# Optimization experiments

Hardware: AMD Instinct MI355X
Metric: run time of the kernel (lower is better)

The kernel has to match this reference:

```python
import jax, jax.numpy as jnp
import numpy as np

INF = 1e6  # stands in for +infinity in the distance transform (fp32-safe when squared)


def _edt(sites):
    """Exact Euclidean distance to the nearest True pixel.
    sites: bool [N, H, W] -> float32 [N, H, W].
    Pass 1: exact 1D distance along width via min-plus cumulative scans.
    Pass 2: lower envelope over rows, d2[y] = min_y' (g[y']^2 + (y-y')^2),
    computed row-by-row with lax.map to avoid an [N,H,W,H] intermediate.
    """
    N, H, W = sites.shape
    pen = jnp.where(sites, 0.0, INF).astype(jnp.float32)  # 0 at sites, INF elsewhere
    xs = jnp.arange(W, dtype=jnp.float32)
    # d_fwd[i] = min_{j<=i} (i - j + pen[j]);  d_bwd[i] = min_{j>=i} (j - i + pen[j])
    fwd = xs + jax.lax.cummin(pen - xs, axis=2)
    bwd = -xs + jax.lax.cummin(pen + xs, axis=2, reverse=True)
    g = jnp.minimum(fwd, bwd)  # exact 1D distance along width
    g2 = g * g
    ys = jnp.arange(H, dtype=jnp.float32)

    def row_min(y):
        # min over source row y' of g2[:, y', :] + (y - y')^2  -> [N, W]
        return jnp.min(g2 + ((y - ys) ** 2)[None, :, None], axis=1)

    d2 = jax.lax.map(row_min, ys)  # [H, N, W]
    return jnp.sqrt(jnp.transpose(d2, (1, 0, 2)))


def _phi(mask):
    """Signed level-set function: -dist_inside on foreground, +dist_outside on background.
    mask: bool [B, H, W]. Images with empty foreground get all-zero phi (as in the torch code).
    """
    sites = jnp.concatenate([~mask, mask], axis=0)  # nearest-background / nearest-foreground
    d = _edt(sites)
    B = mask.shape[0]
    din, dout = d[:B], d[B:]
    phi = jnp.where(mask, -din, dout)
    phi = jnp.where(jnp.abs(phi) > 1e5, 0.0, phi)  # guard degenerate (no-site) cases
    any_fg = jnp.any(mask, axis=(1, 2))
    return jnp.where(any_fg[:, None, None], phi, 0.0)


def setup_inputs() -> dict:
    key = jax.random.key(0)
    k1, k2 = jax.random.split(key)
    predictions = jax.random.normal(k1, (16, 1, 512, 512), dtype=jnp.float32)
    targets = jax.random.randint(k2, (16, 1, 512, 512), 0, 2, dtype=jnp.int32)
    return {"predictions": predictions, "targets": targets}


def reference(predictions, targets):
    alpha = 0.01      # initial_alpha, 'rebalance' schedule at epoch 0
    smooth = 1e-6
    p = jax.nn.sigmoid(predictions)
    t = targets.astype(jnp.float32)
    # Dice loss
    inter = jnp.sum(p * t)
    dice = 1.0 - (2.0 * inter + smooth) / (jnp.sum(p) + jnp.sum(t) + smooth)
    # Boundary loss
    phi = _phi(targets[:, 0].astype(bool))[:, None]  # [B,1,H,W]
    boundary = jnp.mean(phi * p)
    return (1.0 - alpha) * dice + alpha * boundary
```

## Files before the change

### kernel.cpp

```cpp
#include <hip/hip_runtime.h>


#define HH 512
#define WW 512
#define BH 32
#define HALO 16
#define TR 64
#define NT 512
#define NBLK 256
#define SENT 65535.0f

__device__ float fallback_exact(const int* __restrict__ t, int n, int y, int x,
                                bool fg, float m2) {
    const int* tn = t + (n << 18);
    for (int yy = 0; yy < HH; ++yy) {
        float dy = (float)(yy - y);
        float dy2 = dy * dy;
        if (dy2 >= m2) continue;
        const int* row = tn + (yy << 9);
        int lim = (int)sqrtf(m2 - dy2);
        for (int dx = 0; dx <= lim; ++dx) {
            bool hit = false;
            int xl = x - dx, xr = x + dx;
            if (xl >= 0) { int v = row[xl]; hit = fg ? (v == 0) : (v != 0); }
            if (!hit && xr < WW) { int v = row[xr]; hit = fg ? (v == 0) : (v != 0); }
            if (hit) {
                float c = fmaf((float)dx, (float)dx, dy2);
                if (c < m2) m2 = c;
                break;
            }
        }
    }
    return m2;
}

__global__ __launch_bounds__(NT, 1) void edt_fused(const int* __restrict__ t,
                                                   const float* __restrict__ pred,
                                                   double* __restrict__ partials) {
    __shared__ unsigned int gl[TR][WW];
    __shared__ double sred[8][4];

    const int n     = blockIdx.x >> 4;
    const int y0    = (blockIdx.x & 15) << 5;
    const int rbase = y0 - HALO;
    const int wave  = threadIdx.x >> 6;
    const int lane  = threadIdx.x & 63;
    const int x0    = lane << 3;
    const float BIG = 3.0e37f;

    for (int rr = wave; rr < TR; rr += 8) {
        const int gy = rbase + rr;
        if (gy < 0 || gy >= HH) {
            uint4 s = {0xFFFFFFFFu, 0xFFFFFFFFu, 0xFFFFFFFFu, 0xFFFFFFFFu};
            *((uint4*)&gl[rr][x0])     = s;
            *((uint4*)&gl[rr][x0 + 4]) = s;
            continue;
        }
        const int4* tp = (const int4*)(t + (n << 18) + (gy << 9) + x0);
        int4 ta = tp[0], tb = tp[1];
        int tv[8] = {ta.x, ta.y, ta.z, ta.w, tb.x, tb.y, tb.z, tb.w};

        float pen[2][8];
#pragma unroll
        for (int i = 0; i < 8; ++i) {
            bool fg = (tv[i] != 0);
            pen[0][i] = fg ? 1.0e6f : 0.0f;
            pen[1][i] = fg ? 0.0f : 1.0e6f;
        }

        unsigned short gout[2][8];
#pragma unroll
        for (int f = 0; f < 2; ++f) {
            float pf[8];
            float run = BIG;
#pragma unroll
            for (int i = 0; i < 8; ++i) { run = fminf(run, pen[f][i] - (float)(x0 + i)); pf[i] = run; }
            float incl = run;
#pragma unroll
            for (int off = 1; off < 64; off <<= 1) {
                float u = __shfl_up(incl, (unsigned)off, 64);
                if (lane >= off) incl = fminf(incl, u);
            }
            float excl = __shfl_up(incl, 1u, 64);
            if (lane == 0) excl = BIG;

            float sf[8];
            run = BIG;
#pragma unroll
            for (int i = 7; i >= 0; --i) { run = fminf(run, pen[f][i] + (float)(x0 + i)); sf[i] = run; }
            float inclb = run;
#pragma unroll
            for (int off = 1; off < 64; off <<= 1) {
                float u = __shfl_down(inclb, (unsigned)off, 64);
                if (lane + off < 64) inclb = fminf(inclb, u);
            }
            float exclb = __shfl_down(inclb, 1u, 64);
            if (lane == 63) exclb = BIG;

#pragma unroll
            for (int i = 0; i < 8; ++i) {
                float xa = (float)(x0 + i);
                float fa = xa + fminf(pf[i], excl);
                float ba = -xa + fminf(sf[i], exclb);
                gout[f][i] = (unsigned short)fminf(fminf(fa, ba), SENT);
            }
        }

        unsigned int pk[8];
#pragma unroll
        for (int i = 0; i < 8; ++i)
            pk[i] = (unsigned int)gout[0][i] | ((unsigned int)gout[1][i] << 16);
        uint4 o0 = {pk[0], pk[1], pk[2], pk[3]};
        uint4 o1 = {pk[4], pk[5], pk[6], pk[7]};
        *((uint4*)&gl[rr][x0])     = o0;
        *((uint4*)&gl[rr][x0 + 4]) = o1;
    }
    __syncthreads();

    double s_b = 0.0, s_p = 0.0, s_i = 0.0;
    int s_t = 0;

#pragma unroll 1
    for (int grp = 0; grp < 8; ++grp) {
        const int pid = (grp * NT + threadIdx.x) << 2;
        const int yl  = pid >> 9;
        const int x   = pid & 511;
        const int r   = yl + HALO;

        const float4 p4 = *((const float4*)(pred + (n << 18) + ((y0 + yl) << 9) + x));
        const float pv[4] = {p4.x, p4.y, p4.z, p4.w};

        const uint4 ow = *((const uint4*)&gl[r][x]);
        const unsigned int w[4] = {ow.x, ow.y, ow.z, ow.w};

        bool  fg[4];
        float m2[4];
        float mx = 0.0f;
#pragma unroll
        for (int j = 0; j < 4; ++j) {
            unsigned int lo = w[j] & 0xFFFFu, hi = w[j] >> 16;
            fg[j] = (hi == 0u);
            float gv = (float)(fg[j] ? lo : hi);
            m2[j] = gv * gv;
            mx = fmaxf(mx, m2[j]);
        }

        for (int k = 1; k <= HALO; ++k) {
            float k2 = (float)(k * k);
            if (k2 >= mx) break;
            const uint4 wd4 = *((const uint4*)&gl[r - k][x]);
            const uint4 wu4 = *((const uint4*)&gl[r + k][x]);
            const unsigned int wd[4] = {wd4.x, wd4.y, wd4.z, wd4.w};
            const unsigned int wu[4] = {wu4.x, wu4.y, wu4.z, wu4.w};
            mx = 0.0f;
#pragma unroll
            for (int j = 0; j < 4; ++j) {
                if (k2 < m2[j]) {
                    unsigned int a = fg[j] ? (wd[j] & 0xFFFFu) : (wd[j] >> 16);
                    unsigned int b = fg[j] ? (wu[j] & 0xFFFFu) : (wu[j] >> 16);
                    float fa = (float)a, fb = (float)b;
                    m2[j] = fminf(m2[j], fminf(fmaf(fa, fa, k2), fmaf(fb, fb, k2)));
                }
                mx = fmaxf(mx, m2[j]);
            }
        }

        if (mx > 289.0f) {
#pragma unroll
            for (int j = 0; j < 4; ++j)
                if (m2[j] > 289.0f)
                    m2[j] = fallback_exact(t, n, y0 + yl, x + j, fg[j], m2[j]);
        }

#pragma unroll
        for (int j = 0; j < 4; ++j) {
            float p = 1.0f / (1.0f + expf(-pv[j]));
            float d = sqrtf(m2[j]);
            float phi = fg[j] ? -d : d;
            if (d > 1.0e4f) phi = 0.0f;
            s_b += (double)(phi * p);
            s_p += (double)p;
            if (fg[j]) { s_i += (double)p; s_t += 1; }
        }
    }
    double s_tt = (double)s_t;

#pragma unroll
    for (int off = 32; off > 0; off >>= 1) {
        s_b  += __shfl_xor(s_b,  off, 64);
        s_p  += __shfl_xor(s_p,  off, 64);
        s_i  += __shfl_xor(s_i,  off, 64);
        s_tt += __shfl_xor(s_tt, off, 64);
    }
    if (lane == 0) {
        sred[wave][0] = s_b; sred[wave][1] = s_p; sred[wave][2] = s_i; sred[wave][3] = s_tt;
    }
    __syncthreads();
    if (threadIdx.x == 0) {
        double* dst = partials + (size_t)blockIdx.x * 4;
#pragma unroll
        for (int c = 0; c < 4; ++c) {
            double acc = 0.0;
#pragma unroll
            for (int wv = 0; wv < 8; ++wv) acc += sred[wv][c];
            dst[c] = acc;
        }
    }
}

__global__ __launch_bounds__(256) void finalize_loss(const double* __restrict__ partials,
                                                     float* __restrict__ out) {
    const int wave = threadIdx.x >> 6;
    const int lane = threadIdx.x & 63;
    const double* src = partials + (size_t)threadIdx.x * 4;
    double s0 = src[0], s1 = src[1], s2 = src[2], s3 = src[3];
#pragma unroll
    for (int off = 32; off > 0; off >>= 1) {
        s0 += __shfl_xor(s0, off, 64);
        s1 += __shfl_xor(s1, off, 64);
        s2 += __shfl_xor(s2, off, 64);
        s3 += __shfl_xor(s3, off, 64);
    }
    __shared__ double red[4][4];
    if (lane == 0) { red[wave][0] = s0; red[wave][1] = s1; red[wave][2] = s2; red[wave][3] = s3; }
    __syncthreads();
    if (threadIdx.x == 0) {
        double sb = red[0][0] + red[1][0] + red[2][0] + red[3][0];
        double sp = red[0][1] + red[1][1] + red[2][1] + red[3][1];
        double si = red[0][2] + red[1][2] + red[2][2] + red[3][2];
        double st = red[0][3] + red[1][3] + red[2][3] + red[3][3];
        double dice = 1.0 - (2.0 * si + 1e-6) / (sp + st + 1e-6);
        double boundary = sb / (double)(16 * 512 * 512);
        out[0] = (float)(0.99 * dice + 0.01 * boundary);
    }
}

extern "C" void kernel_launch(void* const* d_in, const int* in_sizes, int n_in,
                              void* d_out, int out_size, void* d_ws, size_t ws_size,
                              hipStream_t stream) {
    const float* pred = (const float*)d_in[0];
    const int*   targ = (const int*)d_in[1];
    double* partials = (double*)d_ws;
    float* out = (float*)d_out;

    edt_fused<<<NBLK, NT, 0, stream>>>(targ, pred, partials);
    finalize_loss<<<1, 256, 0, stream>>>(partials, out);
}
```

Baseline: 93.89 us.

## Replace float scan EDT row pass with bitmask clz/ctz and byte-packed distances

Builds a per-row bitmask of the target in shared memory and computes each pixel's horizontal distance to the opposite class with clz/ctz over a 64-bit window, storing a 6-bit distance plus a class bit in one byte instead of two 16-bit values. The row-envelope pass then runs on integer math over the byte-packed table. Shared memory shrinks, and the tile drops to 16 rows with 512 blocks and launch bounds allowing several blocks per CU, which raises occupancy but repeats the 16-row halo work more often. Distances are capped at 63 within a ±24 window, so more pixels may hit the exact fallback path, which is now restarted from scratch.

```diff
diff --git a/kernel.cpp b/kernel.cpp
--- a/kernel.cpp
+++ b/kernel.cpp
@@ -3,12 +3,12 @@
 
 #define HH 512
 #define WW 512
-#define BH 32
+#define BH 16
 #define HALO 16
-#define TR 64
+#define TR 48
 #define NT 512
-#define NBLK 256
-#define SENT 65535.0f
+#define NBLK 512
+#define NGRP 4
 
 __device__ float fallback_exact(const int* __restrict__ t, int n, int y, int x,
                                 bool fg, float m2) {
@@ -19,6 +19,7 @@
         if (dy2 >= m2) continue;
         const int* row = tn + (yy << 9);
         int lim = (int)sqrtf(m2 - dy2);
+        if (lim > WW) lim = WW;
         for (int dx = 0; dx <= lim; ++dx) {
             bool hit = false;
             int xl = x - dx, xr = x + dx;
@@ -34,86 +35,71 @@
     return m2;
 }
 
-__global__ __launch_bounds__(NT, 1) void edt_fused(const int* __restrict__ t,
+__global__ __launch_bounds__(NT, 4) void edt_fused(const int* __restrict__ t,
                                                    const float* __restrict__ pred,
                                                    double* __restrict__ partials) {
-    __shared__ unsigned int gl[TR][WW];
+    __shared__ unsigned long long msk[TR][8];
+    __shared__ unsigned char gb[TR][WW];
     __shared__ double sred[8][4];
 
-    const int n     = blockIdx.x >> 4;
-    const int y0    = (blockIdx.x & 15) << 5;
+    const int n     = blockIdx.x >> 5;
+    const int y0    = (blockIdx.x & 31) << 4;
     const int rbase = y0 - HALO;
     const int wave  = threadIdx.x >> 6;
     const int lane  = threadIdx.x & 63;
     const int x0    = lane << 3;
-    const float BIG = 3.0e37f;
 
     for (int rr = wave; rr < TR; rr += 8) {
         const int gy = rbase + rr;
-        if (gy < 0 || gy >= HH) {
-            uint4 s = {0xFFFFFFFFu, 0xFFFFFFFFu, 0xFFFFFFFFu, 0xFFFFFFFFu};
-            *((uint4*)&gl[rr][x0])     = s;
-            *((uint4*)&gl[rr][x0 + 4]) = s;
-            continue;
-        }
+        if (gy < 0 || gy >= HH) continue;
         const int4* tp = (const int4*)(t + (n << 18) + (gy << 9) + x0);
         int4 ta = tp[0], tb = tp[1];
-        int tv[8] = {ta.x, ta.y, ta.z, ta.w, tb.x, tb.y, tb.z, tb.w};
-
-        float pen[2][8];
-#pragma unroll
-        for (int i = 0; i < 8; ++i) {
-            bool fg = (tv[i] != 0);
-            pen[0][i] = fg ? 1.0e6f : 0.0f;
-            pen[1][i] = fg ? 0.0f : 1.0e6f;
-        }
-
-        unsigned short gout[2][8];
-#pragma unroll
-        for (int f = 0; f < 2; ++f) {
-            float pf[8];
-            float run = BIG;
-#pragma unroll
-            for (int i = 0; i < 8; ++i) { run = fminf(run, pen[f][i] - (float)(x0 + i)); pf[i] = run; }
-            float incl = run;
-#pragma unroll
-            for (int off = 1; off < 64; off <<= 1) {
-                float u = __shfl_up(incl, (unsigned)off, 64);
-                if (lane >= off) incl = fminf(incl, u);
+        unsigned int byte = 0;
+        byte |= (unsigned int)(ta.x != 0) << 0;
+        byte |= (unsigned int)(ta.y != 0) << 1;
+        byte |= (unsigned int)(ta.z != 0) << 2;
+        byte |= (unsigned int)(ta.w != 0) << 3;
+        byte |= (unsigned int)(tb.x != 0) << 4;
+        byte |= (unsigned int)(tb.y != 0) << 5;
+        byte |= (unsigned int)(tb.z != 0) << 6;
+        byte |= (unsigned int)(tb.w != 0) << 7;
+        ((unsigned char*)&msk[rr][0])[lane] = (unsigned char)byte;
+    }
+    __syncthreads();
+
+    {
+        const int s  = (lane - 3) << 3;
+        const int sh = s & 63;
+        const int j0 = s >> 6;
+        unsigned long long V = ~0ull;
+        if (s < 0)   V &= (~0ull) << (-s);
+        if (s > 448) V &= (~0ull) >> (s - 448);
+
+        for (int rr = wave; rr < TR; rr += 8) {
+            const int gy = rbase + rr;
+            unsigned long long pk;
+            if (gy < 0 || gy >= HH) {
+                pk = 0xBFBFBFBFBFBFBFBFull;
+            } else {
+                unsigned long long w0 = (j0 >= 0) ? msk[rr][j0] : 0ull;
+                unsigned long long w1 = (j0 < 7) ? msk[rr][j0 + 1] : 0ull;
+                unsigned long long win = sh ? ((w0 >> sh) | (w1 << (64 - sh))) : w0;
+                pk = 0ull;
+#pragma unroll
+                for (int i = 0; i < 8; ++i) {
+                    const int c = 24 + i;
+                    unsigned int b = (unsigned int)(win >> c) & 1u;
+                    unsigned long long mm = (b ? ~win : win) & V;
+                    unsigned long long lo = mm & ((1ull << c) - 1ull);
+                    unsigned long long hi = mm >> (c + 1);
+                    int dl = lo ? (c - 63 + __builtin_clzll(lo)) : 64;
+                    int dr = hi ? (1 + (int)__builtin_ctzll(hi)) : 64;
+                    int g = min(min(dl, dr), 63);
+                    pk |= ((unsigned long long)((b << 6) | (unsigned int)g)) << (i * 8);
+                }
             }
-            float excl = __shfl_up(incl, 1u, 64);
-            if (lane == 0) excl = BIG;
-
-            float sf[8];
-            run = BIG;
-#pragma unroll
-            for (int i = 7; i >= 0; --i) { run = fminf(run, pen[f][i] + (float)(x0 + i)); sf[i] = run; }
-            float inclb = run;
-#pragma unroll
-            for (int off = 1; off < 64; off <<= 1) {
-                float u = __shfl_down(inclb, (unsigned)off, 64);
-                if (lane + off < 64) inclb = fminf(inclb, u);
-            }
-            float exclb = __shfl_down(inclb, 1u, 64);
-            if (lane == 63) exclb = BIG;
-
-#pragma unroll
-            for (int i = 0; i < 8; ++i) {
-                float xa = (float)(x0 + i);
-                float fa = xa + fminf(pf[i], excl);
-                float ba = -xa + fminf(sf[i], exclb);
-                gout[f][i] = (unsigned short)fminf(fminf(fa, ba), SENT);
-            }
-        }
-
-        unsigned int pk[8];
-#pragma unroll
-        for (int i = 0; i < 8; ++i)
-            pk[i] = (unsigned int)gout[0][i] | ((unsigned int)gout[1][i] << 16);
-        uint4 o0 = {pk[0], pk[1], pk[2], pk[3]};
-        uint4 o1 = {pk[4], pk[5], pk[6], pk[7]};
-        *((uint4*)&gl[rr][x0])     = o0;
-        *((uint4*)&gl[rr][x0 + 4]) = o1;
+            *((unsigned long long*)&gb[rr][x0]) = pk;
+        }
     }
     __syncthreads();
 
@@ -121,7 +107,7 @@
     int s_t = 0;
 
 #pragma unroll 1
-    for (int grp = 0; grp < 8; ++grp) {
+    for (int grp = 0; grp < NGRP; ++grp) {
         const int pid = (grp * NT + threadIdx.x) << 2;
         const int yl  = pid >> 9;
         const int x   = pid & 511;
@@ -130,54 +116,58 @@
         const float4 p4 = *((const float4*)(pred + (n << 18) + ((y0 + yl) << 9) + x));
         const float pv[4] = {p4.x, p4.y, p4.z, p4.w};
 
-        const uint4 ow = *((const uint4*)&gl[r][x]);
-        const unsigned int w[4] = {ow.x, ow.y, ow.z, ow.w};
-
-        bool  fg[4];
-        float m2[4];
-        float mx = 0.0f;
+        const unsigned int ow = *((const unsigned int*)&gb[r][x]);
+        int  m2[4], wc[4];
+        bool fg[4];
+        int  mx = 0;
 #pragma unroll
         for (int j = 0; j < 4; ++j) {
-            unsigned int lo = w[j] & 0xFFFFu, hi = w[j] >> 16;
-            fg[j] = (hi == 0u);
-            float gv = (float)(fg[j] ? lo : hi);
-            m2[j] = gv * gv;
-            mx = fmaxf(mx, m2[j]);
+            unsigned int bj  = (ow >> (8 * j)) & 255u;
+            unsigned int cls = bj >> 6;
+            int gg = (int)(bj & 63u);
+            fg[j] = (cls == 1u);
+            wc[j] = fg[j] ? 0 : 1;
+            m2[j] = gg * gg;
+            mx = max(mx, m2[j]);
         }
 
         for (int k = 1; k <= HALO; ++k) {
-            float k2 = (float)(k * k);
+            const int k2 = k * k;
             if (k2 >= mx) break;
-            const uint4 wd4 = *((const uint4*)&gl[r - k][x]);
-            const uint4 wu4 = *((const uint4*)&gl[r + k][x]);
-            const unsigned int wd[4] = {wd4.x, wd4.y, wd4.z, wd4.w};
-            const unsigned int wu[4] = {wu4.x, wu4.y, wu4.z, wu4.w};
-            mx = 0.0f;
+            const unsigned int bd = *((const unsigned int*)&gb[r - k][x]);
+            const unsigned int bu = *((const unsigned int*)&gb[r + k][x]);
+            mx = 0;
 #pragma unroll
             for (int j = 0; j < 4; ++j) {
                 if (k2 < m2[j]) {
-                    unsigned int a = fg[j] ? (wd[j] & 0xFFFFu) : (wd[j] >> 16);
-                    unsigned int b = fg[j] ? (wu[j] & 0xFFFFu) : (wu[j] >> 16);
-                    float fa = (float)a, fb = (float)b;
-                    m2[j] = fminf(m2[j], fminf(fmaf(fa, fa, k2), fmaf(fb, fb, k2)));
+                    unsigned int dj = (bd >> (8 * j)) & 255u;
+                    unsigned int uj = (bu >> (8 * j)) & 255u;
+                    int a = ((int)(dj >> 6) == wc[j]) ? 0 : (int)(dj & 63u);
+                    int b = ((int)(uj >> 6) == wc[j]) ? 0 : (int)(uj & 63u);
+                    m2[j] = min(m2[j], min(a * a + k2, b * b + k2));
                 }
-                mx = fmaxf(mx, m2[j]);
+                mx = max(mx, m2[j]);
             }
         }
 
-        if (mx > 289.0f) {
+        float df[4];
+#pragma unroll
+        for (int j = 0; j < 4; ++j) df[j] = sqrtf((float)m2[j]);
+
+        if (mx > 289) {
 #pragma unroll
             for (int j = 0; j < 4; ++j)
-                if (m2[j] > 289.0f)
-                    m2[j] = fallback_exact(t, n, y0 + yl, x + j, fg[j], m2[j]);
+                if (m2[j] > 289) {
+                    float fm2 = fallback_exact(t, n, y0 + yl, x + j, fg[j], 1.0e12f);
+                    df[j] = sqrtf(fm2);
+                }
         }
 
 #pragma unroll
         for (int j = 0; j < 4; ++j) {
             float p = 1.0f / (1.0f + expf(-pv[j]));
-            float d = sqrtf(m2[j]);
-            float phi = fg[j] ? -d : d;
-            if (d > 1.0e4f) phi = 0.0f;
+            float phi = fg[j] ? -df[j] : df[j];
+            if (df[j] > 1.0e4f) phi = 0.0f;
             s_b += (double)(phi * p);
             s_p += (double)p;
             if (fg[j]) { s_i += (double)p; s_t += 1; }
@@ -208,7 +198,7 @@
     }
 }
 
-__global__ __launch_bounds__(256) void finalize_loss(const double* __restrict__ partials,
+__global__ __launch_bounds__(512) void finalize_loss(const double* __restrict__ partials,
                                                      float* __restrict__ out) {
     const int wave = threadIdx.x >> 6;
     const int lane = threadIdx.x & 63;
@@ -221,14 +211,15 @@
         s2 += __shfl_xor(s2, off, 64);
         s3 += __shfl_xor(s3, off, 64);
     }
-    __shared__ double red[4][4];
+    __shared__ double red[8][4];
     if (lane == 0) { red[wave][0] = s0; red[wave][1] = s1; red[wave][2] = s2; red[wave][3] = s3; }
     __syncthreads();
     if (threadIdx.x == 0) {
-        double sb = red[0][0] + red[1][0] + red[2][0] + red[3][0];
-        double sp = red[0][1] + red[1][1] + red[2][1] + red[3][1];
-        double si = red[0][2] + red[1][2] + red[2][2] + red[3][2];
-        double st = red[0][3] + red[1][3] + red[2][3] + red[3][3];
+        double sb = 0.0, sp = 0.0, si = 0.0, st = 0.0;
+#pragma unroll
+        for (int wv = 0; wv < 8; ++wv) {
+            sb += red[wv][0]; sp += red[wv][1]; si += red[wv][2]; st += red[wv][3];
+        }
         double dice = 1.0 - (2.0 * si + 1e-6) / (sp + st + 1e-6);
         double boundary = sb / (double)(16 * 512 * 512);
         out[0] = (float)(0.99 * dice + 0.01 * boundary);
@@ -244,5 +235,5 @@
     float* out = (float*)d_out;
 
     edt_fused<<<NBLK, NT, 0, stream>>>(targ, pred, partials);
-    finalize_loss<<<1, 256, 0, stream>>>(partials, out);
-}
+    finalize_loss<<<1, 512, 0, stream>>>(partials, out);
+}
```

Measured after the change: 97.94 us. +4.3%, slower.
